# Performance work log

Measured on AMD Instinct MI355X. Metric: run time of the kernel, lower is better.

The kernel has to match this reference:

```python
import jax, jax.numpy as jnp
import numpy as np

L, E, D = 4, 512, 256   # layers, model dim (=2*D bidirectional), per-direction hidden
T, B = 100, 1000
EPS = 1e-5

def _layernorm(x, g, b):
    m = x.mean(-1, keepdims=True)
    v = x.var(-1, keepdims=True)
    return (x - m) / jnp.sqrt(v + EPS) * g + b

def _dir_scan(U, vf, vr, bf, br):
    # U: (T, B, 4, D) pre-projected gates; SRU elementwise recurrence over time.
    def step(c, u):
        f = jax.nn.sigmoid(u[:, 1] + vf * c + bf)
        c2 = f * c + (1.0 - f) * u[:, 0]
        r = jax.nn.sigmoid(u[:, 2] + vr * c2 + br)
        h = r * c2 + (1.0 - r) * u[:, 3]   # highway with projected residual u3
        return c2, h
    c0 = jnp.zeros((U.shape[1], U.shape[-1]), U.dtype)
    _, H = jax.lax.scan(step, c0, U)
    return H

def setup_inputs() -> dict:
    key = jax.random.key(0)
    ks = jax.random.split(key, 6)
    return {
        "sentence": jax.random.normal(ks[0], (T, B, E), jnp.float32),
        "sru_W": jax.random.normal(ks[1], (L, 2, E, 4 * D), jnp.float32) / np.float32(np.sqrt(E)),
        "sru_v": jax.random.normal(ks[2], (L, 2, 2, D), jnp.float32) * 0.05,
        "sru_b": jnp.zeros((L, 2, 2, D), jnp.float32),
        "ln_g": jnp.ones((L, E), jnp.float32),
        "ln_b": jnp.zeros((L, E), jnp.float32),
        "W1": jax.random.normal(ks[3], (E, E), jnp.float32) / np.float32(np.sqrt(E)),
        "b1": jnp.zeros((E,), jnp.float32),
        "bn_g": jnp.ones((E,), jnp.float32),
        "bn_b": jnp.zeros((E,), jnp.float32),
        "bn_mean": jnp.zeros((E,), jnp.float32),
        "bn_var": jnp.ones((E,), jnp.float32),
        "W2": jax.random.normal(ks[4], (E, 4), jnp.float32) / np.float32(np.sqrt(E)),
        "b2": jnp.zeros((4,), jnp.float32),
    }

def reference(sentence, sru_W, sru_v, sru_b, ln_g, ln_b, W1, b1, bn_g, bn_b, bn_mean, bn_var, W2, b2):
    x = sentence  # (T, B, E)
    for l in range(L):
        xl = _layernorm(x, ln_g[l], ln_b[l])
        # batched projection for both directions: (2, T, B, 4, D)
        U = jnp.einsum('tbi,dik->dtbk', xl, sru_W[l]).reshape(2, T, B, 4, D)
        Hf = _dir_scan(U[0], sru_v[l, 0, 0], sru_v[l, 0, 1], sru_b[l, 0, 0], sru_b[l, 0, 1])
        Hb = _dir_scan(U[1][::-1], sru_v[l, 1, 0], sru_v[l, 1, 1], sru_b[l, 1, 0], sru_b[l, 1, 1])[::-1]
        x = jnp.concatenate([Hf, Hb], axis=-1)  # (T, B, E)
    # head on flattened tokens (eval mode: dropout off, BN uses running stats)
    h = x.reshape(-1, E) @ W1 + b1
    h = (h - bn_mean) / jnp.sqrt(bn_var + EPS) * bn_g + bn_b
    h = jax.nn.relu(h)
    logits = h @ W2 + b2  # (T*B, 4)
    return jax.nn.log_softmax(logits, axis=-1)
```

## Files before the change

### kernel.cpp

```cpp
#include <hip/hip_runtime.h>
#include <stdint.h>

#define T_DIM 100
#define B_DIM 1000
#define E_DIM 512
#define D_DIM 256
#define L_DIM 4
#define M_TOK (T_DIM * B_DIM)
#define M_PAD 100096
#define K_DIM 512
#define MT_NUM (M_PAD / 256)

typedef unsigned short u16;
typedef __bf16 bf16x8 __attribute__((ext_vector_type(8)));
typedef float f32x4 __attribute__((ext_vector_type(4)));
typedef unsigned short ushort8 __attribute__((ext_vector_type(8)));

__device__ __forceinline__ u16 f2bf(float f) {
  unsigned int u = __builtin_bit_cast(unsigned int, f);
  u += 0x7fffu + ((u >> 16) & 1u);
  return (u16)(u >> 16);
}
__device__ __forceinline__ float bf2f(u16 h) {
  unsigned int u = ((unsigned int)h) << 16;
  return __builtin_bit_cast(float, u);
}

__device__ __forceinline__ void gld16(const u16* g, u16* l) {
  __builtin_amdgcn_global_load_lds(
      (const __attribute__((address_space(1))) unsigned int*)g,
      (__attribute__((address_space(3))) unsigned int*)l, 16, 0, 0);
}

__global__ void transpose_cast(const float* __restrict__ in, u16* __restrict__ out,
                               int R, int C) {
  __shared__ float t[32][33];
  const int s = blockIdx.z;
  const float* ib = in + (size_t)s * R * C;
  u16* ob = out + (size_t)s * R * C;
  const int c0 = blockIdx.x * 32, r0 = blockIdx.y * 32;
  const int tx = threadIdx.x, ty = threadIdx.y;
#pragma unroll
  for (int j = 0; j < 4; ++j)
    t[ty + j * 8][tx] = ib[(size_t)(r0 + ty + j * 8) * C + c0 + tx];
  __syncthreads();
#pragma unroll
  for (int j = 0; j < 4; ++j)
    ob[(size_t)(c0 + ty + j * 8) * R + r0 + tx] = f2bf(t[tx][ty + j * 8]);
}

__global__ __launch_bounds__(256) void zero_pad(u16* __restrict__ xl) {
  const int i = blockIdx.x * 256 + threadIdx.x;
  ushort8 z = {0, 0, 0, 0, 0, 0, 0, 0};
  *(ushort8*)(xl + (size_t)M_TOK * 512 + (size_t)i * 8) = z;
}

template <typename TI>
__global__ __launch_bounds__(256) void ln_cast_kernel(
    const TI* __restrict__ x, const float* __restrict__ g,
    const float* __restrict__ b, u16* __restrict__ out) {
  const int wid = threadIdx.x >> 6, lane = threadIdx.x & 63;
  const int row = blockIdx.x * 4 + wid;
  float xe[8];
  if constexpr (sizeof(TI) == 4) {
    const float* xr = (const float*)x + (size_t)row * E_DIM + lane * 8;
    const float4 a = *(const float4*)xr;
    const float4 c = *(const float4*)(xr + 4);
    xe[0] = a.x; xe[1] = a.y; xe[2] = a.z; xe[3] = a.w;
    xe[4] = c.x; xe[5] = c.y; xe[6] = c.z; xe[7] = c.w;
  } else {
    const u16* xr = (const u16*)x + (size_t)row * E_DIM + lane * 8;
    const ushort8 hv = *(const ushort8*)xr;
#pragma unroll
    for (int u = 0; u < 8; ++u) xe[u] = bf2f(hv[u]);
  }
  float s = 0.f, q = 0.f;
#pragma unroll
  for (int u = 0; u < 8; ++u) { s += xe[u]; q += xe[u] * xe[u]; }
#pragma unroll
  for (int off = 32; off; off >>= 1) {
    s += __shfl_xor(s, off, 64);
    q += __shfl_xor(q, off, 64);
  }
  const float mean = s * (1.0f / 512.0f);
  const float var = q * (1.0f / 512.0f) - mean * mean;
  const float rstd = rsqrtf(var + 1e-5f);
  const float4 g0 = *(const float4*)(g + lane * 8);
  const float4 g1 = *(const float4*)(g + lane * 8 + 4);
  const float4 b0 = *(const float4*)(b + lane * 8);
  const float4 b1v = *(const float4*)(b + lane * 8 + 4);
  float ge[8] = {g0.x, g0.y, g0.z, g0.w, g1.x, g1.y, g1.z, g1.w};
  float be[8] = {b0.x, b0.y, b0.z, b0.w, b1v.x, b1v.y, b1v.z, b1v.w};
  ushort8 o;
#pragma unroll
  for (int u = 0; u < 8; ++u)
    o[u] = f2bf((xe[u] - mean) * rstd * ge[u] + be[u]);
  *(ushort8*)(out + (size_t)row * E_DIM + lane * 8) = o;
}

__global__ __launch_bounds__(512, 2) void gemm256(
    const u16* __restrict__ A, const u16* __restrict__ B, u16* __restrict__ C,
    int N, int nc_shift, int ncol_shift) {
  __shared__ u16 As[4][8192];
  __shared__ u16 Bs[4][8192];

  const int bid = blockIdx.x;
  const int xcd = bid & 7;
  const int kk = bid >> 3;
  const int cix = kk & ((1 << nc_shift) - 1);
  const int jj = kk >> nc_shift;
  const int mt = xcd + 8 * jj;
  if (mt >= MT_NUM) return;
  const int z = cix >> ncol_shift;
  const int n0 = (cix & ((1 << ncol_shift) - 1)) << 8;

  const int tid = threadIdx.x;
  const int wave = tid >> 6, lane = tid & 63;
  const int wm = wave >> 2, wn = wave & 3;

  const int r_l = lane >> 2;
  const int c_ld = (lane & 3) ^ ((lane >> 3) & 3);
  const u16* Ag = A + ((size_t)mt * 256 + wave * 32 + r_l) * K_DIM + c_ld * 8;
  const u16* Bg = B + ((size_t)z * N + n0 + wave * 32 + r_l) * K_DIM + c_ld * 8;

  auto STAGE = [&](int t) {
    u16* al = &As[t & 3][wave * 1024];
    u16* bl = &Bs[t & 3][wave * 1024];
    const u16* ag = Ag + t * 32;
    const u16* bg = Bg + t * 32;
    gld16(ag, al);
    gld16(ag + 16 * K_DIM, al + 512);
    gld16(bg, bl);
    gld16(bg + 16 * K_DIM, bl + 512);
  };

  STAGE(0);
  STAGE(1);
  STAGE(2);

  f32x4 acc[8][4] = {};
  const int rA = lane & 15;
  const int sw = ((lane >> 4) ^ ((rA >> 1) & 3)) * 8;
  const int offA = (wm * 128 + rA) * 32 + sw;
  const int offB = (wn * 64 + rA) * 32 + sw;

#pragma unroll
  for (int t = 0; t < 16; ++t) {
    if (t < 14)
      asm volatile("s_waitcnt vmcnt(8) lgkmcnt(0)" ::: "memory");
    else if (t == 14)
      asm volatile("s_waitcnt vmcnt(4) lgkmcnt(0)" ::: "memory");
    else
      asm volatile("s_waitcnt vmcnt(0) lgkmcnt(0)" ::: "memory");
    __builtin_amdgcn_s_barrier();
    asm volatile("" ::: "memory");

    const u16* Ab = As[t & 3];
    const u16* Bb = Bs[t & 3];
    bf16x8 bfr[4], af[4];
#pragma unroll
    for (int fn = 0; fn < 4; ++fn)
      bfr[fn] = *(const bf16x8*)&Bb[offB + fn * 512];
#pragma unroll
    for (int fm = 0; fm < 4; ++fm)
      af[fm] = *(const bf16x8*)&Ab[offA + fm * 512];
    if (t + 3 < 16) STAGE(t + 3);
    __builtin_amdgcn_s_setprio(1);
#pragma unroll
    for (int fm = 0; fm < 4; ++fm)
#pragma unroll
      for (int fn = 0; fn < 4; ++fn)
        acc[fm][fn] = __builtin_amdgcn_mfma_f32_16x16x32_bf16(
            af[fm], bfr[fn], acc[fm][fn], 0, 0, 0);
    __builtin_amdgcn_s_setprio(0);
#pragma unroll
    for (int fm = 0; fm < 4; ++fm)
      af[fm] = *(const bf16x8*)&Ab[offA + (fm + 4) * 512];
    __builtin_amdgcn_s_setprio(1);
#pragma unroll
    for (int fm = 0; fm < 4; ++fm)
#pragma unroll
      for (int fn = 0; fn < 4; ++fn)
        acc[fm + 4][fn] = __builtin_amdgcn_mfma_f32_16x16x32_bf16(
            af[fm], bfr[fn], acc[fm + 4][fn], 0, 0, 0);
    __builtin_amdgcn_s_setprio(0);
  }

  u16* Cb = C + (size_t)z * M_PAD * N;
  const int rr = (lane >> 4) * 4;
  const int cc = lane & 15;
#pragma unroll
  for (int fm = 0; fm < 8; ++fm)
#pragma unroll
    for (int fn = 0; fn < 4; ++fn) {
      const size_t row = (size_t)mt * 256 + wm * 128 + fm * 16 + rr;
      const int col = n0 + wn * 64 + fn * 16 + cc;
#pragma unroll
      for (int r = 0; r < 4; ++r)
        Cb[(row + r) * N + col] = f2bf(acc[fm][fn][r]);
    }
}

__global__ __launch_bounds__(256) void sru_scan(const u16* __restrict__ U,
                                                const float* __restrict__ v,
                                                const float* __restrict__ bb,
                                                u16* __restrict__ xout) {
  const int d = threadIdx.x;
  const int b = blockIdx.x;
  const int dir = blockIdx.y;
  const float vf = v[(dir * 2 + 0) * 256 + d];
  const float vr = v[(dir * 2 + 1) * 256 + d];
  const float bf = bb[(dir * 2 + 0) * 256 + d];
  const float br = bb[(dir * 2 + 1) * 256 + d];
  const u16* Ud = U + (size_t)dir * M_PAD * 1024;
  float c = 0.f;
  for (int s = 0; s < T_DIM; ++s) {
    const int t = dir ? (T_DIM - 1 - s) : s;
    const size_t base = ((size_t)t * B_DIM + b) * 1024 + d;
    const float u0 = bf2f(Ud[base]);
    const float u1 = bf2f(Ud[base + 256]);
    const float u2 = bf2f(Ud[base + 512]);
    const float u3 = bf2f(Ud[base + 768]);
    const float f = 1.f / (1.f + __expf(-(u1 + vf * c + bf)));
    c = f * c + (1.f - f) * u0;
    const float r = 1.f / (1.f + __expf(-(u2 + vr * c + br)));
    const float h = r * c + (1.f - r) * u3;
    xout[((size_t)t * B_DIM + b) * 512 + dir * 256 + d] = f2bf(h);
  }
}

__global__ __launch_bounds__(256) void head_kernel(
    const u16* __restrict__ h, const float* __restrict__ b1,
    const float* __restrict__ bn_g, const float* __restrict__ bn_b,
    const float* __restrict__ bn_mean, const float* __restrict__ bn_var,
    const float* __restrict__ W2, const float* __restrict__ b2,
    float* __restrict__ out) {
  const int wid = threadIdx.x >> 6, lane = threadIdx.x & 63;
  const int row = blockIdx.x * 4 + wid;
  const u16* hr = h + (size_t)row * E_DIM + lane * 8;
  const ushort8 hv = *(const ushort8*)hr;
  float s0 = 0.f, s1 = 0.f, s2 = 0.f, s3 = 0.f;
  const int j0 = lane * 8;
#pragma unroll
  for (int u = 0; u < 8; ++u) {
    const int j = j0 + u;
    const float hb = bf2f(hv[u]) + b1[j];
    float hn = (hb - bn_mean[j]) * rsqrtf(bn_var[j] + 1e-5f) * bn_g[j] + bn_b[j];
    hn = fmaxf(hn, 0.f);
    const float4 w = *(const float4*)(W2 + j * 4);
    s0 += hn * w.x; s1 += hn * w.y; s2 += hn * w.z; s3 += hn * w.w;
  }
#pragma unroll
  for (int off = 32; off; off >>= 1) {
    s0 += __shfl_xor(s0, off, 64);
    s1 += __shfl_xor(s1, off, 64);
    s2 += __shfl_xor(s2, off, 64);
    s3 += __shfl_xor(s3, off, 64);
  }
  if (lane == 0) {
    const float4 bv = *(const float4*)b2;
    const float l0 = s0 + bv.x, l1 = s1 + bv.y, l2 = s2 + bv.z, l3 = s3 + bv.w;
    const float mx = fmaxf(fmaxf(l0, l1), fmaxf(l2, l3));
    const float lse =
        mx + logf(__expf(l0 - mx) + __expf(l1 - mx) + __expf(l2 - mx) + __expf(l3 - mx));
    float4 o = {l0 - lse, l1 - lse, l2 - lse, l3 - lse};
    *(float4*)(out + (size_t)row * 4) = o;
  }
}

extern "C" void kernel_launch(void* const* d_in, const int* in_sizes, int n_in,
                              void* d_out, int out_size, void* d_ws, size_t ws_size,
                              hipStream_t stream) {
  const float* sentence = (const float*)d_in[0];
  const float* sru_W = (const float*)d_in[1];
  const float* sru_v = (const float*)d_in[2];
  const float* sru_b = (const float*)d_in[3];
  const float* ln_g = (const float*)d_in[4];
  const float* ln_b = (const float*)d_in[5];
  const float* W1 = (const float*)d_in[6];
  const float* b1 = (const float*)d_in[7];
  const float* bn_g = (const float*)d_in[8];
  const float* bn_b = (const float*)d_in[9];
  const float* bn_mean = (const float*)d_in[10];
  const float* bn_var = (const float*)d_in[11];
  const float* W2 = (const float*)d_in[12];
  const float* b2 = (const float*)d_in[13];

  char* ws = (char*)d_ws;
  const size_t XL_OFF = 0;
  const size_t X_OFF = XL_OFF + (size_t)M_PAD * 512 * 2;
  const size_t U_OFF = X_OFF + (size_t)M_TOK * 512 * 2;
  const size_t WT_OFF = U_OFF + (size_t)2 * M_PAD * 1024 * 2;
  const size_t W1T_OFF = WT_OFF + (size_t)8 * 512 * 1024 * 2;
  u16* xl = (u16*)(ws + XL_OFF);
  u16* x_buf = (u16*)(ws + X_OFF);
  u16* U = (u16*)(ws + U_OFF);
  u16* WT = (u16*)(ws + WT_OFF);
  u16* W1T = (u16*)(ws + W1T_OFF);
  u16* hbuf = U;

  transpose_cast<<<dim3(32, 16, 8), dim3(32, 8), 0, stream>>>(sru_W, WT, 512, 1024);
  transpose_cast<<<dim3(16, 16, 1), dim3(32, 8), 0, stream>>>(W1, W1T, 512, 512);
  zero_pad<<<24, 256, 0, stream>>>(xl);

  for (int l = 0; l < L_DIM; ++l) {
    if (l == 0)
      ln_cast_kernel<float><<<M_TOK / 4, 256, 0, stream>>>(
          sentence, ln_g, ln_b, xl);
    else
      ln_cast_kernel<u16><<<M_TOK / 4, 256, 0, stream>>>(
          x_buf, ln_g + l * 512, ln_b + l * 512, xl);
    gemm256<<<dim3(8 * 8 * 49), 512, 0, stream>>>(
        xl, WT + (size_t)l * 2 * 1024 * 512, U, 1024, 3, 2);
    u16* xo = (l == L_DIM - 1) ? xl : x_buf;
    sru_scan<<<dim3(1000, 2), 256, 0, stream>>>(U, sru_v + l * 1024,
                                                sru_b + l * 1024, xo);
  }
  gemm256<<<dim3(8 * 2 * 49), 512, 0, stream>>>(xl, W1T, hbuf, 512, 1, 1);
  head_kernel<<<M_TOK / 4, 256, 0, stream>>>(hbuf, b1, bn_g, bn_b, bn_mean,
                                             bn_var, W2, b2, (float*)d_out);
}
```

Baseline: 2.308 ms.

## Split A/B tile prefetch across MFMA phases with finer-grained barriers

The bf16 GEMM main loop now issues the A-tile and B-tile global-to-LDS prefetches separately, each in a different half of the iteration. Each half runs a group of MFMAs between added s_barrier and sched_barrier points, and the vmcnt wait moves to the end of the iteration. The goal is to interleave memory traffic with matrix-core work more evenly across waves and keep LDS reads from stalling the MFMA stream. The cost is more barriers per iteration and hand-tuned wait counts that must stay in step with the number of loads in flight.

```diff
diff --git a/kernel.cpp b/kernel.cpp
--- a/kernel.cpp
+++ b/kernel.cpp
@@ -123,20 +123,22 @@
   const u16* Ag = A + ((size_t)mt * 256 + wave * 32 + r_l) * K_DIM + c_ld * 8;
   const u16* Bg = B + ((size_t)z * N + n0 + wave * 32 + r_l) * K_DIM + c_ld * 8;
 
-  auto STAGE = [&](int t) {
+  auto STAGE_A = [&](int t) {
     u16* al = &As[t & 3][wave * 1024];
-    u16* bl = &Bs[t & 3][wave * 1024];
     const u16* ag = Ag + t * 32;
-    const u16* bg = Bg + t * 32;
     gld16(ag, al);
     gld16(ag + 16 * K_DIM, al + 512);
+  };
+  auto STAGE_B = [&](int t) {
+    u16* bl = &Bs[t & 3][wave * 1024];
+    const u16* bg = Bg + t * 32;
     gld16(bg, bl);
     gld16(bg + 16 * K_DIM, bl + 512);
   };
 
-  STAGE(0);
-  STAGE(1);
-  STAGE(2);
+  STAGE_A(0); STAGE_B(0);
+  STAGE_A(1); STAGE_B(1);
+  STAGE_A(2); STAGE_B(2);
 
   f32x4 acc[8][4] = {};
   const int rA = lane & 15;
@@ -144,46 +146,56 @@
   const int offA = (wm * 128 + rA) * 32 + sw;
   const int offB = (wn * 64 + rA) * 32 + sw;
 
+  asm volatile("s_waitcnt vmcnt(8)" ::: "memory");
+  asm volatile("s_barrier" ::: "memory");
+
 #pragma unroll
   for (int t = 0; t < 16; ++t) {
-    if (t < 14)
-      asm volatile("s_waitcnt vmcnt(8) lgkmcnt(0)" ::: "memory");
-    else if (t == 14)
-      asm volatile("s_waitcnt vmcnt(4) lgkmcnt(0)" ::: "memory");
-    else
-      asm volatile("s_waitcnt vmcnt(0) lgkmcnt(0)" ::: "memory");
-    __builtin_amdgcn_s_barrier();
-    asm volatile("" ::: "memory");
-
     const u16* Ab = As[t & 3];
     const u16* Bb = Bs[t & 3];
-    bf16x8 bfr[4], af[4];
+
+    bf16x8 af0[4], bfr[4];
+#pragma unroll
+    for (int fm = 0; fm < 4; ++fm)
+      af0[fm] = *(const bf16x8*)&Ab[offA + fm * 512];
 #pragma unroll
     for (int fn = 0; fn < 4; ++fn)
       bfr[fn] = *(const bf16x8*)&Bb[offB + fn * 512];
-#pragma unroll
-    for (int fm = 0; fm < 4; ++fm)
-      af[fm] = *(const bf16x8*)&Ab[offA + fm * 512];
-    if (t + 3 < 16) STAGE(t + 3);
+    if (t + 3 < 16) STAGE_A(t + 3);
+    asm volatile("s_barrier" ::: "memory");
+    __builtin_amdgcn_sched_barrier(0);
     __builtin_amdgcn_s_setprio(1);
 #pragma unroll
     for (int fm = 0; fm < 4; ++fm)
 #pragma unroll
       for (int fn = 0; fn < 4; ++fn)
         acc[fm][fn] = __builtin_amdgcn_mfma_f32_16x16x32_bf16(
-            af[fm], bfr[fn], acc[fm][fn], 0, 0, 0);
+            af0[fm], bfr[fn], acc[fm][fn], 0, 0, 0);
     __builtin_amdgcn_s_setprio(0);
+    asm volatile("s_barrier" ::: "memory");
+
+    bf16x8 af1[4];
 #pragma unroll
     for (int fm = 0; fm < 4; ++fm)
-      af[fm] = *(const bf16x8*)&Ab[offA + (fm + 4) * 512];
+      af1[fm] = *(const bf16x8*)&Ab[offA + (fm + 4) * 512];
+    if (t + 3 < 16) STAGE_B(t + 3);
+    asm volatile("s_barrier" ::: "memory");
+    __builtin_amdgcn_sched_barrier(0);
     __builtin_amdgcn_s_setprio(1);
 #pragma unroll
     for (int fm = 0; fm < 4; ++fm)
 #pragma unroll
       for (int fn = 0; fn < 4; ++fn)
         acc[fm + 4][fn] = __builtin_amdgcn_mfma_f32_16x16x32_bf16(
-            af[fm], bfr[fn], acc[fm + 4][fn], 0, 0, 0);
+            af1[fm], bfr[fn], acc[fm + 4][fn], 0, 0, 0);
     __builtin_amdgcn_s_setprio(0);
+    if (t <= 12)
+      asm volatile("s_waitcnt vmcnt(8)" ::: "memory");
+    else if (t == 13)
+      asm volatile("s_waitcnt vmcnt(4)" ::: "memory");
+    else if (t == 14)
+      asm volatile("s_waitcnt vmcnt(0)" ::: "memory");
+    if (t < 15) asm volatile("s_barrier" ::: "memory");
   }
 
   u16* Cb = C + (size_t)z * M_PAD * N;
```

After: 2.309 ms. Within noise of the previous version (+0.1%).
